# Kernel tuning notes

Hardware: AMD Instinct MI355X
Metric: run time of the kernel (lower is better)

Reference implementation:

```python
import math
import jax, jax.numpy as jnp
import numpy as np

PH, PW = 16, 16
MAPPER_X = [0, 0, 6, 0, 0, 1, 1, 4, 5, 1, 3, 0, 0, 0, 3, 2]
MAPPER_Y = [0, 1, 0, 5, 2, 0, 2, 0, 0, 6, 0, 4, 6, 3, 5, 2]


def _make_dct_bases(ph, pw, mapper_x, mapper_y):
    bases = []
    for u, v in zip(mapper_x, mapper_y):
        Bu = np.cos(np.pi * (np.arange(ph) + 0.5) * u / ph) / math.sqrt(ph)
        if u != 0:
            Bu = Bu * math.sqrt(2)
        Bv = np.cos(np.pi * (np.arange(pw) + 0.5) * v / pw) / math.sqrt(pw)
        if v != 0:
            Bv = Bv * math.sqrt(2)
        bases.append(np.outer(Bu, Bv))
    return jnp.asarray(np.stack(bases, axis=0), dtype=jnp.float32)  # [M, ph, pw]


def setup_inputs() -> dict:
    key = jax.random.key(0)
    x = jax.random.normal(key, (16, 64, 224, 224), dtype=jnp.float32)
    dct_bases = _make_dct_bases(PH, PW, MAPPER_X, MAPPER_Y)
    return {"x": x, "dct_bases": dct_bases}


def reference(x, dct_bases):
    # x: [B, C, H, W]; dct_bases: [M, ph, pw]
    B, C, H, W = x.shape
    M, ph, pw = dct_bases.shape
    # H, W chosen divisible by ph, pw -> pad_h = pad_w = 0 (faithful to the no-pad path)
    Hp, Wp = H // ph, W // pw
    x_mean = x.mean(axis=1)                              # [B, H, W]
    patches = x_mean.reshape(B, Hp, ph, Wp, pw)          # non-overlapping unfold
    coeff = jnp.einsum('bhiwj,mij->bmhw', patches, dct_bases)  # [B, M, Hp, Wp]
    # nearest upsample by (ph, pw): broadcast each coeff over its patch footprint
    freq = jnp.broadcast_to(coeff[:, :, :, None, :, None], (B, M, Hp, ph, Wp, pw))
    return freq.reshape(B, M, H, W)
```

## Files before the change

### kernel.cpp

```cpp
#include <hip/hip_runtime.h>

#define B_  16
#define C_  64
#define H_  224
#define W_  224
#define M_  16
#define PH  16
#define PW  16
#define HP  14
#define WP  14

__global__ __launch_bounds__(256)
void dct_patch_fused(const float* __restrict__ x,
                     const float* __restrict__ bases,
                     float* __restrict__ out) {
    const int bid = blockIdx.x;
    const int wp  = bid % WP;
    const int hp  = (bid / WP) % HP;
    const int b   = bid / (WP * HP);

    __shared__ float4 part[256];
    __shared__ float  meanp[PH * 17];
    __shared__ float  coef[M_];

    const int t  = threadIdx.x;
    const int f4 = t & 63;
    const int cg = t >> 6;
    const int i  = f4 >> 2;
    const int c4 = f4 & 3;

    const size_t plane = (size_t)H_ * W_;

    const float* p = x + ((size_t)b * C_ + (size_t)cg * 16) * plane
                       + (size_t)(hp * PH + i) * W_ + (size_t)(wp * PW + c4 * 4);
    float4 acc = {0.f, 0.f, 0.f, 0.f};
#pragma unroll
    for (int cc = 0; cc < 16; ++cc) {
        float4 v = *(const float4*)(p + (size_t)cc * plane);
        acc.x += v.x; acc.y += v.y; acc.z += v.z; acc.w += v.w;
    }
    part[t] = acc;
    __syncthreads();

    if (t < 64) {
        float4 a0 = part[t];
        float4 a1 = part[t + 64];
        float4 a2 = part[t + 128];
        float4 a3 = part[t + 192];
        const float inv = 1.f / (float)C_;
        meanp[i * 17 + c4 * 4 + 0] = (a0.x + a1.x + a2.x + a3.x) * inv;
        meanp[i * 17 + c4 * 4 + 1] = (a0.y + a1.y + a2.y + a3.y) * inv;
        meanp[i * 17 + c4 * 4 + 2] = (a0.z + a1.z + a2.z + a3.z) * inv;
        meanp[i * 17 + c4 * 4 + 3] = (a0.w + a1.w + a2.w + a3.w) * inv;
    }
    __syncthreads();

    {
        const int m = t >> 4;
        const int s = t & 15;
        const float* brow = bases + (size_t)m * (PH * PW) + (size_t)s * PW;
        float partial = 0.f;
#pragma unroll
        for (int k = 0; k < 16; ++k)
            partial += meanp[s * 17 + k] * brow[k];
        partial += __shfl_xor(partial, 1);
        partial += __shfl_xor(partial, 2);
        partial += __shfl_xor(partial, 4);
        partial += __shfl_xor(partial, 8);
        if (s == 0) coef[m] = partial;
    }
    __syncthreads();

    {
        const int m = t >> 4;
        const int r = t & 15;
        const float cv = coef[m];
        float4 v4 = {cv, cv, cv, cv};
        float* op = out + ((size_t)b * M_ + m) * plane
                        + (size_t)(hp * PH + r) * W_ + (size_t)(wp * PW);
        *(float4*)(op + 0)  = v4;
        *(float4*)(op + 4)  = v4;
        *(float4*)(op + 8)  = v4;
        *(float4*)(op + 12) = v4;
    }
}

extern "C" void kernel_launch(void* const* d_in, const int* in_sizes, int n_in,
                              void* d_out, int out_size, void* d_ws, size_t ws_size,
                              hipStream_t stream) {
    const float* x     = (const float*)d_in[0];
    const float* bases = (const float*)d_in[1];
    float* out         = (float*)d_out;

    const int nblocks = B_ * HP * WP;
    dct_patch_fused<<<nblocks, 256, 0, stream>>>(x, bases, out);
}
```

Baseline: 302.9 us.

## Split fused DCT kernel into coalesced mean, coefficient, and broadcast kernels

Replaces the per-patch fused kernel with three kernels: a channel-mean pass reading whole planes contiguously, a small per-patch DCT coefficient kernel, and a broadcast kernel writing the output contiguously. The aim is to replace 64-byte strided row accesses with fully coalesced streaming reads and writes. In exchange it adds a workspace round trip for the mean image and coefficients, two extra launches, and fewer, longer-running threads in the mean pass.

```diff
diff --git a/kernel.cpp b/kernel.cpp
--- a/kernel.cpp
+++ b/kernel.cpp
@@ -1,88 +1,81 @@
 #include <hip/hip_runtime.h>
 
-#define B_  16
-#define C_  64
-#define H_  224
-#define W_  224
-#define M_  16
-#define PH  16
-#define PW  16
-#define HP  14
-#define WP  14
+#define B_   16
+#define C_   64
+#define H_   224
+#define W_   224
+#define M_   16
+#define PH   16
+#define PW   16
+#define HP   14
+#define WP   14
+#define PLANE (H_ * W_)
+#define PLANE4 (PLANE / 4)
+#define NCOEF (B_ * M_ * HP * WP)
 
 __global__ __launch_bounds__(256)
-void dct_patch_fused(const float* __restrict__ x,
-                     const float* __restrict__ bases,
-                     float* __restrict__ out) {
-    const int bid = blockIdx.x;
-    const int wp  = bid % WP;
-    const int hp  = (bid / WP) % HP;
-    const int b   = bid / (WP * HP);
-
-    __shared__ float4 part[256];
-    __shared__ float  meanp[PH * 17];
-    __shared__ float  coef[M_];
-
-    const int t  = threadIdx.x;
-    const int f4 = t & 63;
-    const int cg = t >> 6;
-    const int i  = f4 >> 2;
-    const int c4 = f4 & 3;
-
-    const size_t plane = (size_t)H_ * W_;
-
-    const float* p = x + ((size_t)b * C_ + (size_t)cg * 16) * plane
-                       + (size_t)(hp * PH + i) * W_ + (size_t)(wp * PW + c4 * 4);
+void k1_mean(const float* __restrict__ x, float* __restrict__ mean) {
+    const int f4 = blockIdx.x * 256 + threadIdx.x;
+    const int b  = blockIdx.y;
+    const float4* p = (const float4*)x + (size_t)b * C_ * PLANE4 + f4;
     float4 acc = {0.f, 0.f, 0.f, 0.f};
-#pragma unroll
-    for (int cc = 0; cc < 16; ++cc) {
-        float4 v = *(const float4*)(p + (size_t)cc * plane);
+#pragma unroll 16
+    for (int c = 0; c < C_; ++c) {
+        float4 v = p[(size_t)c * PLANE4];
         acc.x += v.x; acc.y += v.y; acc.z += v.z; acc.w += v.w;
     }
-    part[t] = acc;
-    __syncthreads();
+    const float inv = 1.f / (float)C_;
+    acc.x *= inv; acc.y *= inv; acc.z *= inv; acc.w *= inv;
+    ((float4*)mean)[(size_t)b * PLANE4 + f4] = acc;
+}
 
+__global__ __launch_bounds__(256)
+void k2a_coeff(const float* __restrict__ mean, const float* __restrict__ bases,
+               float* __restrict__ coeff) {
+    const int pid = blockIdx.x;
+    const int wp  = pid % WP;
+    const int hp  = pid / WP;
+    const int b   = blockIdx.y;
+
+    __shared__ float patch[PH * 20];
+
+    const int t = threadIdx.x;
     if (t < 64) {
-        float4 a0 = part[t];
-        float4 a1 = part[t + 64];
-        float4 a2 = part[t + 128];
-        float4 a3 = part[t + 192];
-        const float inv = 1.f / (float)C_;
-        meanp[i * 17 + c4 * 4 + 0] = (a0.x + a1.x + a2.x + a3.x) * inv;
-        meanp[i * 17 + c4 * 4 + 1] = (a0.y + a1.y + a2.y + a3.y) * inv;
-        meanp[i * 17 + c4 * 4 + 2] = (a0.z + a1.z + a2.z + a3.z) * inv;
-        meanp[i * 17 + c4 * 4 + 3] = (a0.w + a1.w + a2.w + a3.w) * inv;
+        const int i  = t >> 2;
+        const int c4 = t & 3;
+        const float4 v = *(const float4*)(mean + (size_t)b * PLANE
+                                          + (size_t)(hp * PH + i) * W_
+                                          + wp * PW + c4 * 4);
+        *(float4*)&patch[i * 20 + c4 * 4] = v;
     }
     __syncthreads();
 
-    {
-        const int m = t >> 4;
-        const int s = t & 15;
-        const float* brow = bases + (size_t)m * (PH * PW) + (size_t)s * PW;
-        float partial = 0.f;
+    const int m = t >> 4;
+    const int s = t & 15;
+    const float* brow = bases + m * (PH * PW) + s * PW;
+    float partial = 0.f;
 #pragma unroll
-        for (int k = 0; k < 16; ++k)
-            partial += meanp[s * 17 + k] * brow[k];
-        partial += __shfl_xor(partial, 1);
-        partial += __shfl_xor(partial, 2);
-        partial += __shfl_xor(partial, 4);
-        partial += __shfl_xor(partial, 8);
-        if (s == 0) coef[m] = partial;
-    }
-    __syncthreads();
+    for (int k = 0; k < 16; ++k)
+        partial += patch[s * 20 + k] * brow[k];
+    partial += __shfl_xor(partial, 1);
+    partial += __shfl_xor(partial, 2);
+    partial += __shfl_xor(partial, 4);
+    partial += __shfl_xor(partial, 8);
+    if (s == 0)
+        coeff[(((size_t)b * M_ + m) * HP + hp) * WP + wp] = partial;
+}
 
-    {
-        const int m = t >> 4;
-        const int r = t & 15;
-        const float cv = coef[m];
-        float4 v4 = {cv, cv, cv, cv};
-        float* op = out + ((size_t)b * M_ + m) * plane
-                        + (size_t)(hp * PH + r) * W_ + (size_t)(wp * PW);
-        *(float4*)(op + 0)  = v4;
-        *(float4*)(op + 4)  = v4;
-        *(float4*)(op + 8)  = v4;
-        *(float4*)(op + 12) = v4;
-    }
+__global__ __launch_bounds__(256)
+void k2b_broadcast(const float* __restrict__ coeff, float* __restrict__ out) {
+    const int o4 = blockIdx.x * 256 + threadIdx.x;
+    const int bm = blockIdx.y;
+    const int w4 = o4 % (W_ / 4);
+    const int h  = o4 / (W_ / 4);
+    const int hp = h >> 4;
+    const int wp = w4 >> 2;
+    const float c = coeff[((size_t)bm * HP + hp) * WP + wp];
+    float4 v = {c, c, c, c};
+    ((float4*)out)[(size_t)bm * PLANE4 + o4] = v;
 }
 
 extern "C" void kernel_launch(void* const* d_in, const int* in_sizes, int n_in,
@@ -92,6 +85,15 @@
     const float* bases = (const float*)d_in[1];
     float* out         = (float*)d_out;
 
-    const int nblocks = B_ * HP * WP;
-    dct_patch_fused<<<nblocks, 256, 0, stream>>>(x, bases, out);
+    float* mean  = (float*)d_ws;
+    float* coeff = mean + (size_t)B_ * PLANE;
+
+    dim3 g1(PLANE4 / 256, B_);
+    k1_mean<<<g1, 256, 0, stream>>>(x, mean);
+
+    dim3 g2(HP * WP, B_);
+    k2a_coeff<<<g2, 256, 0, stream>>>(mean, bases, coeff);
+
+    dim3 g3(PLANE4 / 256, B_ * M_);
+    k2b_broadcast<<<g3, 256, 0, stream>>>(coeff, out);
 }
```

Result: no change. 304.2 us (+0.4%).
